# Performance work log

Hardware: AMD Instinct MI355X
Metric: run time of the kernel (lower is better)

## Reference

```python
import jax, jax.numpy as jnp
import numpy as np

DIM = 512
HEADS = 8
HEAD_DIM = DIM // HEADS
FFN = 1536
WIN = 16
EPS = 1e-6


def rms_norm(x, w):
    var = jnp.mean(x * x, axis=-1, keepdims=True)
    return x * jax.lax.rsqrt(var + EPS) * w


def rotate_half(x):
    x1, x2 = jnp.split(x, 2, axis=-1)
    return jnp.concatenate([-x2, x1], axis=-1)


def apply_rope(q, k, inv_freq, position_ids):
    # q,k: [B,H,S,D]; inv_freq: [D//2]; position_ids: [B,S]
    ang = position_ids[:, :, None].astype(jnp.float32) * inv_freq[None, None, :]  # [B,S,D/2]
    cos = jnp.concatenate([jnp.cos(ang), jnp.cos(ang)], axis=-1)[:, None]  # [B,1,S,D]
    sin = jnp.concatenate([jnp.sin(ang), jnp.sin(ang)], axis=-1)[:, None]
    q = q * cos + rotate_half(q) * sin
    k = k * cos + rotate_half(k) * sin
    return q, k


def setup_inputs() -> dict:
    key = jax.random.key(0)
    ks = jax.random.split(key, 12)
    B, S = 2, 4096
    x = jax.random.normal(ks[0], (B, S, DIM), dtype=jnp.float32)
    inv_freq = 1.0 / (10000.0 ** (jnp.arange(0, HEAD_DIM, 2, dtype=jnp.float32) / HEAD_DIM))  # [D/2]
    position_ids = jnp.broadcast_to(jnp.arange(S, dtype=jnp.int64), (B, S))
    key_padding_mask = jnp.zeros((B, S), dtype=bool)  # True = padded (ignored)
    s = 0.02
    return {
        "x": x,
        "rope_freqs": inv_freq,
        "position_ids": position_ids,
        "key_padding_mask": key_padding_mask,
        "norm1_w": jnp.ones((DIM,), jnp.float32),
        "wq": jax.random.normal(ks[1], (DIM, DIM), jnp.float32) * s,
        "wk": jax.random.normal(ks[2], (DIM, DIM), jnp.float32) * s,
        "wv": jax.random.normal(ks[3], (DIM, DIM), jnp.float32) * s,
        "wo": jax.random.normal(ks[4], (DIM, DIM), jnp.float32) * s,
        "norm2_w": jnp.ones((DIM,), jnp.float32),
        "w1": jax.random.normal(ks[5], (DIM, FFN), jnp.float32) * s,  # gate proj
        "w2": jax.random.normal(ks[6], (DIM, FFN), jnp.float32) * s,  # up proj
        "w3": jax.random.normal(ks[7], (FFN, DIM), jnp.float32) * s,  # down proj
    }


def local_attention(h, rope_freqs, position_ids, key_padding_mask, wq, wk, wv, wo):
    B, S, _ = h.shape
    q = jnp.einsum("bsd,de->bse", h, wq).reshape(B, S, HEADS, HEAD_DIM).transpose(0, 2, 1, 3)
    k = jnp.einsum("bsd,de->bse", h, wk).reshape(B, S, HEADS, HEAD_DIM).transpose(0, 2, 1, 3)
    v = jnp.einsum("bsd,de->bse", h, wv).reshape(B, S, HEADS, HEAD_DIM).transpose(0, 2, 1, 3)
    q, k = apply_rope(q, k, rope_freqs, position_ids)

    offs = jnp.arange(-WIN, WIN + 1)                       # [W]
    pos = jnp.arange(S)[:, None] + offs[None, :]           # [S,W]
    in_range = (pos >= 0) & (pos < S)                      # [S,W]
    pos_c = jnp.clip(pos, 0, S - 1)
    k_band = k[:, :, pos_c]                                # [B,H,S,W,D]
    v_band = v[:, :, pos_c]
    scores = jnp.einsum("bhsd,bhswd->bhsw", q, k_band) * (HEAD_DIM ** -0.5)
    keep = in_range[None, None] & (~key_padding_mask[:, pos_c])[:, None]  # [B,1->H,S,W]
    scores = jnp.where(keep, scores, -1e9)
    attn = jax.nn.softmax(scores, axis=-1)
    out = jnp.einsum("bhsw,bhswd->bhsd", attn, v_band)
    out = out.transpose(0, 2, 1, 3).reshape(B, S, DIM)
    return jnp.einsum("bsd,de->bse", out, wo)


def swiglu(h, w1, w2, w3):
    return jnp.einsum("bsf,fd->bsd", jax.nn.silu(h @ w1) * (h @ w2), w3)


def reference(x, rope_freqs, position_ids, key_padding_mask,
              norm1_w, wq, wk, wv, wo, norm2_w, w1, w2, w3):
    x = x + local_attention(rms_norm(x, norm1_w), rope_freqs, position_ids,
                            key_padding_mask, wq, wk, wv, wo)
    x = x + swiglu(rms_norm(x, norm2_w), w1, w2, w3)
    return x
```

## Files before the change

### kernel.cpp

```cpp
#include <hip/hip_runtime.h>
#include <math.h>

#define DIM   512
#define HEADS 8
#define HD    64
#define FFN_N 1536
#define WIN   16
#define SEQ   4096
#define BAND  (64 + 2 * WIN)
#define LDA   64

#define QKVN  1536

typedef __attribute__((ext_vector_type(8))) short bf16x8;
typedef __attribute__((ext_vector_type(4))) float f32x4;
typedef _Float16 f16;
typedef __attribute__((ext_vector_type(2))) _Float16 f16x2;

__device__ inline unsigned short f2bf(float f) {
  union { float f; unsigned u; } v; v.f = f;
  unsigned r = (v.u + 0x7FFF + ((v.u >> 16) & 1)) >> 16;
  return (unsigned short)r;
}

__device__ __forceinline__ float fast_rcp(float x) {
#if __has_builtin(__builtin_amdgcn_rcpf)
  return __builtin_amdgcn_rcpf(x);
#else
  return 1.0f / x;
#endif
}

__device__ __forceinline__ void gl2lds16(const void* g, void* l) {
  __builtin_amdgcn_global_load_lds(
      (const __attribute__((address_space(1))) unsigned int*)g,
      (__attribute__((address_space(3))) unsigned int*)l, 16, 0, 0);
}

__global__ __launch_bounds__(256) void k_preamble(
    const float* __restrict__ wq, const float* __restrict__ wk, const float* __restrict__ wv,
    const float* __restrict__ wo, const float* __restrict__ w1, const float* __restrict__ w2,
    const float* __restrict__ w3,
    unsigned short* __restrict__ BTqkv, unsigned short* __restrict__ BTwo,
    unsigned short* __restrict__ BTw12, unsigned short* __restrict__ BTw3,
    const float* __restrict__ invf, float* __restrict__ Ct, float* __restrict__ St,
    const float* __restrict__ X, const float* __restrict__ n1w,
    unsigned short* __restrict__ H, int ntok) {
  int bid = blockIdx.x;
  if (bid < 3328) {
    const float* src; unsigned short* dst; int K, N, t;
    if      (bid < 256)  { src = wq; dst = BTqkv;               K = 512;  N = 512;  t = bid; }
    else if (bid < 512)  { src = wk; dst = BTqkv + 512 * 512;   K = 512;  N = 512;  t = bid - 256; }
    else if (bid < 768)  { src = wv; dst = BTqkv + 1024 * 512;  K = 512;  N = 512;  t = bid - 512; }
    else if (bid < 1024) { src = wo; dst = BTwo;                K = 512;  N = 512;  t = bid - 768; }
    else if (bid < 1792) { src = w1; dst = BTw12;               K = 512;  N = 1536; t = bid - 1024; }
    else if (bid < 2560) { src = w2; dst = BTw12 + 1536 * 512;  K = 512;  N = 1536; t = bid - 1792; }
    else                 { src = w3; dst = BTw3;                K = 1536; N = 512;  t = bid - 2560; }
    int ntn = N >> 5;
    int tn = t % ntn, tk = t / ntn;
    __shared__ float T[32][33];
    int r = threadIdx.x >> 3, c = (threadIdx.x & 7) << 2;
    float4 s = *(const float4*)(src + (size_t)(tk * 32 + r) * N + tn * 32 + c);
    T[r][c + 0] = s.x; T[r][c + 1] = s.y; T[r][c + 2] = s.z; T[r][c + 3] = s.w;
    __syncthreads();
    ushort4 o = make_ushort4(f2bf(T[c + 0][r]), f2bf(T[c + 1][r]), f2bf(T[c + 2][r]), f2bf(T[c + 3][r]));
    *(ushort4*)(dst + (size_t)(tn * 32 + r) * K + tk * 32 + c) = o;
  } else if (bid < 3840) {
    int idx = (bid - 3328) * 256 + threadIdx.x;
    int p = idx & 31;
    int s = idx >> 5;
    float ang = (float)s * invf[p];
    float sn, cs;
    __sincosf(ang, &sn, &cs);
    Ct[idx] = cs;
    St[idx] = sn;
  } else {
    int wave = (bid - 3840) * 4 + (threadIdx.x >> 6);
    if (wave >= ntok) return;
    int lane = threadIdx.x & 63;
    const float* x = X + (size_t)wave * DIM;
    float4 a = *(const float4*)(x + lane * 4);
    float4 b = *(const float4*)(x + 256 + lane * 4);
    float ss = a.x*a.x + a.y*a.y + a.z*a.z + a.w*a.w
             + b.x*b.x + b.y*b.y + b.z*b.z + b.w*b.w;
#pragma unroll
    for (int off = 32; off; off >>= 1) ss += __shfl_xor(ss, off, 64);
    float r = rsqrtf(ss * (1.0f / DIM) + 1e-6f);
    float4 wa = *(const float4*)(n1w + lane * 4);
    float4 wb = *(const float4*)(n1w + 256 + lane * 4);
    unsigned short* o = H + (size_t)wave * DIM;
    *(ushort4*)(o + lane * 4)       = make_ushort4(f2bf(a.x*r*wa.x), f2bf(a.y*r*wa.y), f2bf(a.z*r*wa.z), f2bf(a.w*r*wa.w));
    *(ushort4*)(o + 256 + lane * 4) = make_ushort4(f2bf(b.x*r*wb.x), f2bf(b.y*r*wb.y), f2bf(b.z*r*wb.z), f2bf(b.w*r*wb.w));
  }
}

__global__ __launch_bounds__(256) void k_rmsnorm(const float* __restrict__ X,
                                                 const float* __restrict__ W,
                                                 unsigned short* __restrict__ O, int ntok) {
  int wave = blockIdx.x * 4 + (threadIdx.x >> 6);
  if (wave >= ntok) return;
  int lane = threadIdx.x & 63;
  const float* x = X + (size_t)wave * DIM;
  float4 a = *(const float4*)(x + lane * 4);
  float4 b = *(const float4*)(x + 256 + lane * 4);
  float ss = a.x*a.x + a.y*a.y + a.z*a.z + a.w*a.w
           + b.x*b.x + b.y*b.y + b.z*b.z + b.w*b.w;
#pragma unroll
  for (int off = 32; off; off >>= 1) ss += __shfl_xor(ss, off, 64);
  float r = rsqrtf(ss * (1.0f / DIM) + 1e-6f);
  float4 wa = *(const float4*)(W + lane * 4);
  float4 wb = *(const float4*)(W + 256 + lane * 4);
  unsigned short* o = O + (size_t)wave * DIM;
  *(ushort4*)(o + lane * 4)       = make_ushort4(f2bf(a.x*r*wa.x), f2bf(a.y*r*wa.y), f2bf(a.z*r*wa.z), f2bf(a.w*r*wa.w));
  *(ushort4*)(o + 256 + lane * 4) = make_ushort4(f2bf(b.x*r*wb.x), f2bf(b.y*r*wb.y), f2bf(b.z*r*wb.z), f2bf(b.w*r*wb.w));
}

__global__ __launch_bounds__(256) void k_mgemm(
    const unsigned short* __restrict__ A, const unsigned short* __restrict__ BT,
    float* __restrict__ C, const float* __restrict__ R, int M, int N, int K) {
  __shared__ __align__(16) unsigned short As[128 * 32];
  __shared__ __align__(16) unsigned short Bs[64 * 32];
  int tid = threadIdx.x;
  int lane = tid & 63, wave = tid >> 6;
  int q4 = lane >> 4, l16 = lane & 15;
  int bM = blockIdx.x, bN = blockIdx.y;

  f32x4 acc[2][4];
#pragma unroll
  for (int i = 0; i < 2; ++i)
#pragma unroll
    for (int j = 0; j < 4; ++j) acc[i][j] = (f32x4){0.f, 0.f, 0.f, 0.f};

  int lrow = lane >> 2;
  int cg   = (((lane & 3) ^ ((lane >> 3) & 3)) << 3);
  unsigned short* AsW0 = As + (wave * 32) * 32;
  unsigned short* AsW1 = As + (wave * 32 + 16) * 32;
  unsigned short* BsW  = Bs + (wave * 16) * 32;
  const unsigned short* Ag0 = A  + (size_t)(bM * 128 + wave * 32 + lrow) * K + cg;
  const unsigned short* Ag1 = Ag0 + (size_t)16 * K;
  const unsigned short* Bg  = BT + (size_t)(bN * 64 + wave * 16 + lrow) * K + cg;

  int xc = ((q4 ^ ((l16 >> 1) & 3)) << 3);

  for (int k0 = 0; k0 < K; k0 += 32) {
    __syncthreads();
    gl2lds16(Ag0 + k0, AsW0);
    gl2lds16(Ag1 + k0, AsW1);
    gl2lds16(Bg  + k0, BsW);
    __syncthreads();
    bf16x8 af[2], bf[4];
#pragma unroll
    for (int mi = 0; mi < 2; ++mi)
      af[mi] = *(const bf16x8*)&As[(wave * 32 + mi * 16 + l16) * 32 + xc];
#pragma unroll
    for (int ni = 0; ni < 4; ++ni)
      bf[ni] = *(const bf16x8*)&Bs[(ni * 16 + l16) * 32 + xc];
#pragma unroll
    for (int mi = 0; mi < 2; ++mi)
#pragma unroll
      for (int ni = 0; ni < 4; ++ni)
        acc[mi][ni] = __builtin_amdgcn_mfma_f32_16x16x32_bf16(af[mi], bf[ni], acc[mi][ni], 0, 0, 0);
  }
#pragma unroll
  for (int mi = 0; mi < 2; ++mi)
#pragma unroll
    for (int ni = 0; ni < 4; ++ni) {
      int col = bN * 64 + ni * 16 + l16;
#pragma unroll
      for (int r = 0; r < 4; ++r) {
        int row = bM * 128 + wave * 32 + mi * 16 + q4 * 4 + r;
        float v = acc[mi][ni][r];
        if (R) v += R[(size_t)row * N + col];
        C[(size_t)row * N + col] = v;
      }
    }
}

__global__ __launch_bounds__(256) void k_mgemm128(
    const unsigned short* __restrict__ A, const unsigned short* __restrict__ BT,
    f16* __restrict__ C, int M, int N, int K) {
  __shared__ __align__(16) unsigned short As[128 * 32];
  __shared__ __align__(16) unsigned short Bs[128 * 32];
  int tid = threadIdx.x;
  int lane = tid & 63, wave = tid >> 6;
  int wm = wave & 1, wn = wave >> 1;
  int q4 = lane >> 4, l16 = lane & 15;
  int bM = blockIdx.x, bN = blockIdx.y;

  f32x4 acc[4][4];
#pragma unroll
  for (int i = 0; i < 4; ++i)
#pragma unroll
    for (int j = 0; j < 4; ++j) acc[i][j] = (f32x4){0.f, 0.f, 0.f, 0.f};

  int lrow = lane >> 2;
  int cg   = (((lane & 3) ^ ((lane >> 3) & 3)) << 3);
  unsigned short* AsW0 = As + (wave * 32) * 32;
  unsigned short* AsW1 = As + (wave * 32 + 16) * 32;
  unsigned short* BsW0 = Bs + (wave * 32) * 32;
  unsigned short* BsW1 = Bs + (wave * 32 + 16) * 32;
  const unsigned short* Ag0 = A  + (size_t)(bM * 128 + wave * 32 + lrow) * K + cg;
  const unsigned short* Ag1 = Ag0 + (size_t)16 * K;
  const unsigned short* Bg0 = BT + (size_t)(bN * 128 + wave * 32 + lrow) * K + cg;
  const unsigned short* Bg1 = Bg0 + (size_t)16 * K;

  int xc = ((q4 ^ ((l16 >> 1) & 3)) << 3);

  for (int k0 = 0; k0 < K; k0 += 32) {
    __syncthreads();
    gl2lds16(Ag0 + k0, AsW0);
    gl2lds16(Ag1 + k0, AsW1);
    gl2lds16(Bg0 + k0, BsW0);
    gl2lds16(Bg1 + k0, BsW1);
    __syncthreads();
    bf16x8 af[4], bf[4];
#pragma unroll
    for (int mi = 0; mi < 4; ++mi)
      af[mi] = *(const bf16x8*)&As[(wm * 64 + mi * 16 + l16) * 32 + xc];
#pragma unroll
    for (int ni = 0; ni < 4; ++ni)
      bf[ni] = *(const bf16x8*)&Bs[(wn * 64 + ni * 16 + l16) * 32 + xc];
#pragma unroll
    for (int mi = 0; mi < 4; ++mi)
#pragma unroll
      for (int ni = 0; ni < 4; ++ni)
        acc[mi][ni] = __builtin_amdgcn_mfma_f32_16x16x32_bf16(af[mi], bf[ni], acc[mi][ni], 0, 0, 0);
  }
#pragma unroll
  for (int mi = 0; mi < 4; ++mi)
#pragma unroll
    for (int ni = 0; ni < 4; ++ni) {
      int col = bN * 128 + wn * 64 + ni * 16 + l16;
#pragma unroll
      for (int r = 0; r < 4; ++r) {
        int row = bM * 128 + wm * 64 + mi * 16 + q4 * 4 + r;
        C[(size_t)row * N + col] = (f16)acc[mi][ni][r];
      }
    }
}

__global__ __launch_bounds__(256) void k_mgemm_swiglu(
    const unsigned short* __restrict__ A, const unsigned short* __restrict__ B1T,
    const unsigned short* __restrict__ B2T, unsigned short* __restrict__ Y,
    int M, int N, int K) {
  __shared__ __align__(16) unsigned short As[128 * 32];
  __shared__ __align__(16) unsigned short B1s[64 * 32];
  __shared__ __align__(16) unsigned short B2s[64 * 32];
  int tid = threadIdx.x;
  int lane = tid & 63, wave = tid >> 6;
  int q4 = lane >> 4, l16 = lane & 15;
  int bM = blockIdx.x, bN = blockIdx.y;

  f32x4 acc[2][2][4];
#pragma unroll
  for (int t = 0; t < 2; ++t)
#pragma unroll
    for (int i = 0; i < 2; ++i)
#pragma unroll
      for (int j = 0; j < 4; ++j) acc[t][i][j] = (f32x4){0.f, 0.f, 0.f, 0.f};

  int lrow = lane >> 2;
  int cg   = (((lane & 3) ^ ((lane >> 3) & 3)) << 3);
  unsigned short* AsW0 = As  + (wave * 32) * 32;
  unsigned short* AsW1 = As  + (wave * 32 + 16) * 32;
  unsigned short* B1sW = B1s + (wave * 16) * 32;
  unsigned short* B2sW = B2s + (wave * 16) * 32;
  const unsigned short* Ag0 = A   + (size_t)(bM * 128 + wave * 32 + lrow) * K + cg;
  const unsigned short* Ag1 = Ag0 + (size_t)16 * K;
  const unsigned short* B1g = B1T + (size_t)(bN * 64 + wave * 16 + lrow) * K + cg;
  const unsigned short* B2g = B2T + (size_t)(bN * 64 + wave * 16 + lrow) * K + cg;

  int xc = ((q4 ^ ((l16 >> 1) & 3)) << 3);

  for (int k0 = 0; k0 < K; k0 += 32) {
    __syncthreads();
    gl2lds16(Ag0 + k0, AsW0);
    gl2lds16(Ag1 + k0, AsW1);
    gl2lds16(B1g + k0, B1sW);
    gl2lds16(B2g + k0, B2sW);
    __syncthreads();
    bf16x8 af[2], b1f[4], b2f[4];
#pragma unroll
    for (int mi = 0; mi < 2; ++mi)
      af[mi] = *(const bf16x8*)&As[(wave * 32 + mi * 16 + l16) * 32 + xc];
#pragma unroll
    for (int ni = 0; ni < 4; ++ni) {
      b1f[ni] = *(const bf16x8*)&B1s[(ni * 16 + l16) * 32 + xc];
      b2f[ni] = *(const bf16x8*)&B2s[(ni * 16 + l16) * 32 + xc];
    }
#pragma unroll
    for (int mi = 0; mi < 2; ++mi)
#pragma unroll
      for (int ni = 0; ni < 4; ++ni) {
        acc[0][mi][ni] = __builtin_amdgcn_mfma_f32_16x16x32_bf16(af[mi], b1f[ni], acc[0][mi][ni], 0, 0, 0);
        acc[1][mi][ni] = __builtin_amdgcn_mfma_f32_16x16x32_bf16(af[mi], b2f[ni], acc[1][mi][ni], 0, 0, 0);
      }
  }
#pragma unroll
  for (int mi = 0; mi < 2; ++mi)
#pragma unroll
    for (int ni = 0; ni < 4; ++ni) {
      int col = bN * 64 + ni * 16 + l16;
#pragma unroll
      for (int r = 0; r < 4; ++r) {
        int row = bM * 128 + wave * 32 + mi * 16 + q4 * 4 + r;
        float g = acc[0][mi][ni][r];
        float u = acc[1][mi][ni][r];
        float yv = g * fast_rcp(1.0f + __expf(-g)) * u;
        Y[(size_t)row * N + col] = f2bf(yv);
      }
    }
}

__global__ __launch_bounds__(128) void k_attn(const f16* __restrict__ QKV,
                                              const float* __restrict__ Ct,
                                              const float* __restrict__ St,
                                              unsigned short* __restrict__ O) {
  __shared__ __align__(16) f16 KV[BAND * LDA];
  int tid = threadIdx.x;
  int c0 = blockIdx.x * 64;
  int h = blockIdx.y, b = blockIdx.z;

#pragma unroll
  for (int base = 0; base < BAND; base += 16) {
    int r  = base + (tid >> 3);
    int c8 = (tid & 7) << 3;
    int sr = c0 - WIN + r;
    int scl = min(max(sr, 0), SEQ - 1);
    const f16* kr = QKV + ((size_t)(b * SEQ + scl)) * QKVN + h * HD + 512;
    int p = c8 & 31;
    union { int4 w; f16 x[8]; } ov, pv, pk;
    ov.w = *(const int4*)(kr + c8);
    pv.w = *(const int4*)(kr + (c8 ^ 32));
    float4 cv0 = *(const float4*)(Ct + scl * 32 + p);
    float4 cv1 = *(const float4*)(Ct + scl * 32 + p + 4);
    float4 sv0 = *(const float4*)(St + scl * 32 + p);
    float4 sv1 = *(const float4*)(St + scl * 32 + p + 4);
    float cs[8] = {cv0.x, cv0.y, cv0.z, cv0.w, cv1.x, cv1.y, cv1.z, cv1.w};
    float sn[8] = {sv0.x, sv0.y, sv0.z, sv0.w, sv1.x, sv1.y, sv1.z, sv1.w};
    float sg = (c8 < 32) ? -1.f : 1.f;
#pragma unroll
    for (int j = 0; j < 8; ++j)
      pk.x[j] = (f16)((float)ov.x[j] * cs[j] + sg * (float)pv.x[j] * sn[j]);
    *(int4*)&KV[r * LDA + ((((c8 >> 3) ^ (r & 7))) << 3)] = pk.w;
  }
  __syncthreads();

  int lane = tid & 63;
  int ql   = (tid >> 6) * 32 + (lane >> 1);
  int half = lane & 1;
  int s    = c0 + ql;

  const f16* qp = QKV + ((size_t)(b * SEQ + s)) * QKVN + h * HD;
  f16x2 qh[16];
  {
    float sg = half ? 1.f : -1.f;
#pragma unroll
    for (int k = 0; k < 4; ++k) {
      union { int4 w; f16 x[8]; } ov, pv;
      ov.w = *(const int4*)(qp + half * 32 + 8 * k);
      pv.w = *(const int4*)(qp + (half ^ 1) * 32 + 8 * k);
      float4 cv0 = *(const float4*)(Ct + (size_t)s * 32 + 8 * k);
      float4 cv1 = *(const float4*)(Ct + (size_t)s * 32 + 8 * k + 4);
      float4 sv0 = *(const float4*)(St + (size_t)s * 32 + 8 * k);
      float4 sv1 = *(const float4*)(St + (size_t)s * 32 + 8 * k + 4);
      float cs[8] = {cv0.x, cv0.y, cv0.z, cv0.w, cv1.x, cv1.y, cv1.z, cv1.w};
      float sn[8] = {sv0.x, sv0.y, sv0.z, sv0.w, sv1.x, sv1.y, sv1.z, sv1.w};
#pragma unroll
      for (int j = 0; j < 4; ++j) {
        float a = (float)ov.x[2 * j]     * cs[2 * j]     + sg * (float)pv.x[2 * j]     * sn[2 * j];
        float c = (float)ov.x[2 * j + 1] * cs[2 * j + 1] + sg * (float)pv.x[2 * j + 1] * sn[2 * j + 1];
        qh[4 * k + j] = (f16x2){(f16)a, (f16)c};
      }
    }
  }

  int jlo = max(s - WIN, 0);
  int nj  = min(s + WIN, SEQ - 1) - jlo + 1;
  int r0  = jlo - (c0 - WIN);

  float sc[33];
#pragma unroll
  for (int t = 0; t < 33; ++t) {
    int rr = r0 + t;
    const f16* kr = &KV[rr * LDA];
    int sw = rr & 7;
    union { int4 w; f16x2 hx[4]; } L[4];
#pragma unroll
    for (int jj = 0; jj < 4; ++jj)
      L[jj].w = *(const int4*)(kr + (((half * 4 + jj) ^ sw) << 3));
    float pa = 0.f, pb = 0.f;
#pragma unroll
    for (int k = 0; k < 4; ++k) {
#if __has_builtin(__builtin_amdgcn_fdot2)
      pa = __builtin_amdgcn_fdot2(qh[4 * k + 0], L[k].hx[0], pa, false);
      pb = __builtin_amdgcn_fdot2(qh[4 * k + 1], L[k].hx[1], pb, false);
      pa = __builtin_amdgcn_fdot2(qh[4 * k + 2], L[k].hx[2], pa, false);
      pb = __builtin_amdgcn_fdot2(qh[4 * k + 3], L[k].hx[3], pb, false);
#else
#pragma unroll
      for (int j = 0; j < 4; ++j) {
        pa += (float)qh[4 * k + j][0] * (float)L[k].hx[j][0];
        pb += (float)qh[4 * k + j][1] * (float)L[k].hx[j][1];
      }
#endif
    }
    float sv = pa + pb;
    sv += __shfl_xor(sv, 1, 64);
    sc[t] = (t < nj) ? sv * 0.125f : -1e30f;
  }
  float m = -1e30f;
#pragma unroll
  for (int t = 0; t < 33; ++t) m = fmaxf(m, sc[t]);
  float sum = 0.f;
#pragma unroll
  for (int t = 0; t < 33; ++t) { float e = __expf(sc[t] - m); sc[t] = e; sum += e; }
  float inv = fast_rcp(sum);

  __syncthreads();

#pragma unroll
  for (int base = 0; base < BAND; base += 16) {
    int r  = base + (tid >> 3);
    int c8 = (tid & 7) << 3;
    int sr = c0 - WIN + r;
    int scl = min(max(sr, 0), SEQ - 1);
    const f16* vr = QKV + ((size_t)(b * SEQ + scl)) * QKVN + h * HD + 1024;
    int4 w = *(const int4*)(vr + c8);
    *(int4*)&KV[r * LDA + ((((c8 >> 3) ^ (r & 7))) << 3)] = w;
  }
  __syncthreads();

  float o[32];
#pragma unroll
  for (int i = 0; i < 32; ++i) o[i] = 0.f;
#pragma unroll
  for (int t = 0; t < 33; ++t) {
    float w = sc[t] * inv;
    int rr = r0 + t;
    const f16* vr = &KV[rr * LDA];
    int sw = rr & 7;
    union { int4 w4; f16 x[8]; } A[4];
#pragma unroll
    for (int jj = 0; jj < 4; ++jj)
      A[jj].w4 = *(const int4*)(vr + (((half * 4 + jj) ^ sw) << 3));
#pragma unroll
    for (int k = 0; k < 4; ++k)
#pragma unroll
      for (int j = 0; j < 8; ++j)
        o[8 * k + j] += w * (float)A[k].x[j];
  }
  unsigned short* op = O + ((size_t)(b * SEQ + s)) * DIM + h * HD + half * 32;
#pragma unroll
  for (int v = 0; v < 4; ++v) {
    union { int4 w; unsigned short u[8]; } pk;
#pragma unroll
    for (int j = 0; j < 8; ++j) pk.u[j] = f2bf(o[8 * v + j]);
    *(int4*)(op + 8 * v) = pk.w;
  }
}

extern "C" void kernel_launch(void* const* d_in, const int* in_sizes, int n_in,
                              void* d_out, int out_size, void* d_ws, size_t ws_size,
                              hipStream_t stream) {
  const float* x    = (const float*)d_in[0];
  const float* invf = (const float*)d_in[1];
  const float* n1w = (const float*)d_in[4];
  const float* wq  = (const float*)d_in[5];
  const float* wk  = (const float*)d_in[6];
  const float* wv  = (const float*)d_in[7];
  const float* wo  = (const float*)d_in[8];
  const float* n2w = (const float*)d_in[9];
  const float* w1  = (const float*)d_in[10];
  const float* w2  = (const float*)d_in[11];
  const float* w3  = (const float*)d_in[12];
  float* out = (float*)d_out;

  const int ntok = in_sizes[0] / DIM;
  const int B    = ntok / SEQ;

  unsigned char* p = (unsigned char*)d_ws;
  f16* QKV = (f16*)p;                        p += (size_t)ntok * QKVN * 2;
  unsigned short* hbf  = (unsigned short*)p; p += (size_t)ntok * DIM * 2;
  unsigned short* aO   = (unsigned short*)p; p += (size_t)ntok * DIM * 2;
  unsigned short* h2   = (unsigned short*)p; p += (size_t)ntok * DIM * 2;
  unsigned short* yb   = (unsigned short*)p; p += (size_t)ntok * FFN_N * 2;
  unsigned short* BTqkv= (unsigned short*)p; p += (size_t)QKVN * DIM * 2;
  unsigned short* BTwo = (unsigned short*)p; p += (size_t)DIM * DIM * 2;
  unsigned short* BTw12= (unsigned short*)p; p += (size_t)2 * FFN_N * DIM * 2;
  unsigned short* BTw3 = (unsigned short*)p; p += (size_t)DIM * FFN_N * 2;
  float* Ct = (float*)p;                     p += (size_t)SEQ * 32 * 4;
  float* St = (float*)p;                     p += (size_t)SEQ * 32 * 4;

  k_preamble<<<3328 + 512 + ntok / 4, 256, 0, stream>>>(
      wq, wk, wv, wo, w1, w2, w3, BTqkv, BTwo, BTw12, BTw3,
      invf, Ct, St, x, n1w, hbf, ntok);
  {
    dim3 g(ntok / 128, QKVN / 128);
    k_mgemm128<<<g, 256, 0, stream>>>(hbf, BTqkv, QKV, ntok, QKVN, DIM);
  }
  {
    dim3 gA(SEQ / 64, HEADS, B);
    k_attn<<<gA, 128, 0, stream>>>(QKV, Ct, St, aO);
  }
  {
    dim3 g(ntok / 128, DIM / 64);
    k_mgemm<<<g, 256, 0, stream>>>(aO, BTwo, out, x, ntok, DIM, DIM);
  }
  k_rmsnorm<<<ntok / 4, 256, 0, stream>>>(out, n2w, h2, ntok);
  {
    dim3 g(ntok / 128, FFN_N / 64);
    k_mgemm_swiglu<<<g, 256, 0, stream>>>(h2, BTw12, BTw12 + (size_t)FFN_N * DIM, yb, ntok, FFN_N, DIM);
  }
  {
    dim3 g(ntok / 128, DIM / 64);
    k_mgemm<<<g, 256, 0, stream>>>(yb, BTw3, out, out, ntok, DIM, FFN_N);
  }
}
```

Baseline: 234.5 us.

## Multi-buffer LDS staging in the three MFMA GEMM kernels

Replaces the single-buffer load/sync/compute loops in the GEMM, 128-tile GEMM and SwiGLU GEMM kernels with a multi-stage LDS ring (4, 3 and 2 buffers), using explicit vmcnt waits plus barriers. The aim is to overlap global-to-LDS async loads with MFMA compute and to cut the per-iteration barrier pair. This costs more LDS per block, which may reduce occupancy. Relying on inline asm vmcnt counts is also fragile: the code assumes a single barrier is enough to avoid overwriting a buffer other waves are still reading.

```diff
diff --git a/kernel.cpp b/kernel.cpp
--- a/kernel.cpp
+++ b/kernel.cpp
@@ -36,6 +36,8 @@
       (const __attribute__((address_space(1))) unsigned int*)g,
       (__attribute__((address_space(3))) unsigned int*)l, 16, 0, 0);
 }
+
+#define WAITBAR(n) asm volatile("s_waitcnt vmcnt(" #n ")\n\ts_barrier" ::: "memory")
 
 __global__ __launch_bounds__(256) void k_preamble(
     const float* __restrict__ wq, const float* __restrict__ wk, const float* __restrict__ wv,
@@ -118,8 +120,8 @@
 __global__ __launch_bounds__(256) void k_mgemm(
     const unsigned short* __restrict__ A, const unsigned short* __restrict__ BT,
     float* __restrict__ C, const float* __restrict__ R, int M, int N, int K) {
-  __shared__ __align__(16) unsigned short As[128 * 32];
-  __shared__ __align__(16) unsigned short Bs[64 * 32];
+  __shared__ __align__(16) unsigned short As[4][128 * 32];
+  __shared__ __align__(16) unsigned short Bs[4][64 * 32];
   int tid = threadIdx.x;
   int lane = tid & 63, wave = tid >> 6;
   int q4 = lane >> 4, l16 = lane & 15;
@@ -133,34 +135,56 @@
 
   int lrow = lane >> 2;
   int cg   = (((lane & 3) ^ ((lane >> 3) & 3)) << 3);
-  unsigned short* AsW0 = As + (wave * 32) * 32;
-  unsigned short* AsW1 = As + (wave * 32 + 16) * 32;
-  unsigned short* BsW  = Bs + (wave * 16) * 32;
+  int aoff0 = (wave * 32) * 32;
+  int aoff1 = (wave * 32 + 16) * 32;
+  int boff  = (wave * 16) * 32;
   const unsigned short* Ag0 = A  + (size_t)(bM * 128 + wave * 32 + lrow) * K + cg;
   const unsigned short* Ag1 = Ag0 + (size_t)16 * K;
   const unsigned short* Bg  = BT + (size_t)(bN * 64 + wave * 16 + lrow) * K + cg;
 
   int xc = ((q4 ^ ((l16 >> 1) & 3)) << 3);
-
-  for (int k0 = 0; k0 < K; k0 += 32) {
-    __syncthreads();
-    gl2lds16(Ag0 + k0, AsW0);
-    gl2lds16(Ag1 + k0, AsW1);
-    gl2lds16(Bg  + k0, BsW);
-    __syncthreads();
-    bf16x8 af[2], bf[4];
-#pragma unroll
-    for (int mi = 0; mi < 2; ++mi)
-      af[mi] = *(const bf16x8*)&As[(wave * 32 + mi * 16 + l16) * 32 + xc];
-#pragma unroll
-    for (int ni = 0; ni < 4; ++ni)
-      bf[ni] = *(const bf16x8*)&Bs[(ni * 16 + l16) * 32 + xc];
-#pragma unroll
-    for (int mi = 0; mi < 2; ++mi)
-#pragma unroll
-      for (int ni = 0; ni < 4; ++ni)
-        acc[mi][ni] = __builtin_amdgcn_mfma_f32_16x16x32_bf16(af[mi], bf[ni], acc[mi][ni], 0, 0, 0);
-  }
+  int nk = K >> 5;
+
+#define MG_STAGE(t_, b_) do {                         \
+    int k0_ = (t_) * 32;                              \
+    gl2lds16(Ag0 + k0_, &As[b_][aoff0]);              \
+    gl2lds16(Ag1 + k0_, &As[b_][aoff1]);              \
+    gl2lds16(Bg  + k0_, &Bs[b_][boff]);               \
+  } while (0)
+
+#define MG_CONSUME(b_) do {                                                        \
+    const unsigned short* Asb = As[b_];                                            \
+    const unsigned short* Bsb = Bs[b_];                                            \
+    bf16x8 af[2], bf[4];                                                           \
+    _Pragma("unroll")                                                              \
+    for (int mi = 0; mi < 2; ++mi)                                                 \
+      af[mi] = *(const bf16x8*)&Asb[(wave * 32 + mi * 16 + l16) * 32 + xc];        \
+    _Pragma("unroll")                                                              \
+    for (int ni = 0; ni < 4; ++ni)                                                 \
+      bf[ni] = *(const bf16x8*)&Bsb[(ni * 16 + l16) * 32 + xc];                    \
+    _Pragma("unroll")                                                              \
+    for (int mi = 0; mi < 2; ++mi)                                                 \
+      _Pragma("unroll")                                                            \
+      for (int ni = 0; ni < 4; ++ni)                                               \
+        acc[mi][ni] = __builtin_amdgcn_mfma_f32_16x16x32_bf16(af[mi], bf[ni],      \
+                                                              acc[mi][ni], 0,0,0); \
+  } while (0)
+
+#pragma unroll
+  for (int t = 0; t < 3; ++t) MG_STAGE(t, t);
+
+  for (int t = 0; t < nk - 2; ++t) {
+    WAITBAR(6);
+    if (t + 3 < nk) MG_STAGE(t + 3, (t + 3) & 3);
+    MG_CONSUME(t & 3);
+  }
+  WAITBAR(3);
+  MG_CONSUME((nk - 2) & 3);
+  WAITBAR(0);
+  MG_CONSUME((nk - 1) & 3);
+#undef MG_STAGE
+#undef MG_CONSUME
+
 #pragma unroll
   for (int mi = 0; mi < 2; ++mi)
 #pragma unroll
@@ -179,8 +203,8 @@
 __global__ __launch_bounds__(256) void k_mgemm128(
     const unsigned short* __restrict__ A, const unsigned short* __restrict__ BT,
     f16* __restrict__ C, int M, int N, int K) {
-  __shared__ __align__(16) unsigned short As[128 * 32];
-  __shared__ __align__(16) unsigned short Bs[128 * 32];
+  __shared__ __align__(16) unsigned short As[3][128 * 32];
+  __shared__ __align__(16) unsigned short Bs[3][128 * 32];
   int tid = threadIdx.x;
   int lane = tid & 63, wave = tid >> 6;
   int wm = wave & 1, wn = wave >> 1;
@@ -195,37 +219,58 @@
 
   int lrow = lane >> 2;
   int cg   = (((lane & 3) ^ ((lane >> 3) & 3)) << 3);
-  unsigned short* AsW0 = As + (wave * 32) * 32;
-  unsigned short* AsW1 = As + (wave * 32 + 16) * 32;
-  unsigned short* BsW0 = Bs + (wave * 32) * 32;
-  unsigned short* BsW1 = Bs + (wave * 32 + 16) * 32;
+  int aoff0 = (wave * 32) * 32;
+  int aoff1 = (wave * 32 + 16) * 32;
   const unsigned short* Ag0 = A  + (size_t)(bM * 128 + wave * 32 + lrow) * K + cg;
   const unsigned short* Ag1 = Ag0 + (size_t)16 * K;
   const unsigned short* Bg0 = BT + (size_t)(bN * 128 + wave * 32 + lrow) * K + cg;
   const unsigned short* Bg1 = Bg0 + (size_t)16 * K;
 
   int xc = ((q4 ^ ((l16 >> 1) & 3)) << 3);
-
-  for (int k0 = 0; k0 < K; k0 += 32) {
-    __syncthreads();
-    gl2lds16(Ag0 + k0, AsW0);
-    gl2lds16(Ag1 + k0, AsW1);
-    gl2lds16(Bg0 + k0, BsW0);
-    gl2lds16(Bg1 + k0, BsW1);
-    __syncthreads();
-    bf16x8 af[4], bf[4];
-#pragma unroll
-    for (int mi = 0; mi < 4; ++mi)
-      af[mi] = *(const bf16x8*)&As[(wm * 64 + mi * 16 + l16) * 32 + xc];
-#pragma unroll
-    for (int ni = 0; ni < 4; ++ni)
-      bf[ni] = *(const bf16x8*)&Bs[(wn * 64 + ni * 16 + l16) * 32 + xc];
-#pragma unroll
-    for (int mi = 0; mi < 4; ++mi)
-#pragma unroll
-      for (int ni = 0; ni < 4; ++ni)
-        acc[mi][ni] = __builtin_amdgcn_mfma_f32_16x16x32_bf16(af[mi], bf[ni], acc[mi][ni], 0, 0, 0);
-  }
+  int nk = K >> 5;
+
+#define MG128_STAGE(t_, b_) do {                      \
+    int k0_ = (t_) * 32;                              \
+    gl2lds16(Ag0 + k0_, &As[b_][aoff0]);              \
+    gl2lds16(Ag1 + k0_, &As[b_][aoff1]);              \
+    gl2lds16(Bg0 + k0_, &Bs[b_][aoff0]);              \
+    gl2lds16(Bg1 + k0_, &Bs[b_][aoff1]);              \
+  } while (0)
+
+#define MG128_CONSUME(b_) do {                                                     \
+    const unsigned short* Asb = As[b_];                                            \
+    const unsigned short* Bsb = Bs[b_];                                            \
+    bf16x8 af[4], bf[4];                                                           \
+    _Pragma("unroll")                                                              \
+    for (int mi = 0; mi < 4; ++mi)                                                 \
+      af[mi] = *(const bf16x8*)&Asb[(wm * 64 + mi * 16 + l16) * 32 + xc];          \
+    _Pragma("unroll")                                                              \
+    for (int ni = 0; ni < 4; ++ni)                                                 \
+      bf[ni] = *(const bf16x8*)&Bsb[(wn * 64 + ni * 16 + l16) * 32 + xc];          \
+    _Pragma("unroll")                                                              \
+    for (int mi = 0; mi < 4; ++mi)                                                 \
+      _Pragma("unroll")                                                            \
+      for (int ni = 0; ni < 4; ++ni)                                               \
+        acc[mi][ni] = __builtin_amdgcn_mfma_f32_16x16x32_bf16(af[mi], bf[ni],      \
+                                                              acc[mi][ni], 0,0,0); \
+  } while (0)
+
+  MG128_STAGE(0, 0);
+  MG128_STAGE(1, 1);
+
+  int cb = 0, sb = 2;
+  for (int t = 0; t < nk - 1; ++t) {
+    WAITBAR(4);
+    if (t + 2 < nk) MG128_STAGE(t + 2, sb);
+    MG128_CONSUME(cb);
+    cb = (cb == 2) ? 0 : cb + 1;
+    sb = (sb == 2) ? 0 : sb + 1;
+  }
+  WAITBAR(0);
+  MG128_CONSUME(cb);
+#undef MG128_STAGE
+#undef MG128_CONSUME
+
 #pragma unroll
   for (int mi = 0; mi < 4; ++mi)
 #pragma unroll
@@ -243,9 +288,9 @@
     const unsigned short* __restrict__ A, const unsigned short* __restrict__ B1T,
     const unsigned short* __restrict__ B2T, unsigned short* __restrict__ Y,
     int M, int N, int K) {
-  __shared__ __align__(16) unsigned short As[128 * 32];
-  __shared__ __align__(16) unsigned short B1s[64 * 32];
-  __shared__ __align__(16) unsigned short B2s[64 * 32];
+  __shared__ __align__(16) unsigned short As[2][128 * 32];
+  __shared__ __align__(16) unsigned short B1s[2][64 * 32];
+  __shared__ __align__(16) unsigned short B2s[2][64 * 32];
   int tid = threadIdx.x;
   int lane = tid & 63, wave = tid >> 6;
   int q4 = lane >> 4, l16 = lane & 15;
@@ -261,32 +306,42 @@
 
   int lrow = lane >> 2;
   int cg   = (((lane & 3) ^ ((lane >> 3) & 3)) << 3);
-  unsigned short* AsW0 = As  + (wave * 32) * 32;
-  unsigned short* AsW1 = As  + (wave * 32 + 16) * 32;
-  unsigned short* B1sW = B1s + (wave * 16) * 32;
-  unsigned short* B2sW = B2s + (wave * 16) * 32;
+  int aoff0 = (wave * 32) * 32;
+  int aoff1 = (wave * 32 + 16) * 32;
+  int boff  = (wave * 16) * 32;
   const unsigned short* Ag0 = A   + (size_t)(bM * 128 + wave * 32 + lrow) * K + cg;
   const unsigned short* Ag1 = Ag0 + (size_t)16 * K;
   const unsigned short* B1g = B1T + (size_t)(bN * 64 + wave * 16 + lrow) * K + cg;
   const unsigned short* B2g = B2T + (size_t)(bN * 64 + wave * 16 + lrow) * K + cg;
 
   int xc = ((q4 ^ ((l16 >> 1) & 3)) << 3);
-
-  for (int k0 = 0; k0 < K; k0 += 32) {
-    __syncthreads();
-    gl2lds16(Ag0 + k0, AsW0);
-    gl2lds16(Ag1 + k0, AsW1);
-    gl2lds16(B1g + k0, B1sW);
-    gl2lds16(B2g + k0, B2sW);
-    __syncthreads();
+  int nk = K >> 5;
+
+#define SW_STAGE(t_, b_) do {                         \
+    int k0_ = (t_) * 32;                              \
+    gl2lds16(Ag0 + k0_, &As[b_][aoff0]);              \
+    gl2lds16(Ag1 + k0_, &As[b_][aoff1]);              \
+    gl2lds16(B1g + k0_, &B1s[b_][boff]);              \
+    gl2lds16(B2g + k0_, &B2s[b_][boff]);              \
+  } while (0)
+
+  SW_STAGE(0, 0);
+
+  for (int t = 0; t < nk; ++t) {
+    WAITBAR(0);
+    if (t + 1 < nk) SW_STAGE(t + 1, (t + 1) & 1);
+    int cb = t & 1;
+    const unsigned short* Asb  = As[cb];
+    const unsigned short* B1sb = B1s[cb];
+    const unsigned short* B2sb = B2s[cb];
     bf16x8 af[2], b1f[4], b2f[4];
 #pragma unroll
     for (int mi = 0; mi < 2; ++mi)
-      af[mi] = *(const bf16x8*)&As[(wave * 32 + mi * 16 + l16) * 32 + xc];
+      af[mi] = *(const bf16x8*)&Asb[(wave * 32 + mi * 16 + l16) * 32 + xc];
 #pragma unroll
     for (int ni = 0; ni < 4; ++ni) {
-      b1f[ni] = *(const bf16x8*)&B1s[(ni * 16 + l16) * 32 + xc];
-      b2f[ni] = *(const bf16x8*)&B2s[(ni * 16 + l16) * 32 + xc];
+      b1f[ni] = *(const bf16x8*)&B1sb[(ni * 16 + l16) * 32 + xc];
+      b2f[ni] = *(const bf16x8*)&B2sb[(ni * 16 + l16) * 32 + xc];
     }
 #pragma unroll
     for (int mi = 0; mi < 2; ++mi)
@@ -296,6 +351,8 @@
         acc[1][mi][ni] = __builtin_amdgcn_mfma_f32_16x16x32_bf16(af[mi], b2f[ni], acc[1][mi][ni], 0, 0, 0);
       }
   }
+#undef SW_STAGE
+
 #pragma unroll
   for (int mi = 0; mi < 2; ++mi)
 #pragma unroll
```

Result: faster. 225.1 us (-4.0%).
